# Kernel optimization log

Hardware: AMD Instinct MI355X
Metric: run time of the kernel (lower is better)

Reference implementation:

```python
import jax, jax.numpy as jnp
import numpy as np

M, N, P, T = 8000, 63, 64, 5


def setup_inputs() -> dict:
    key = jax.random.key(0)
    ks = jax.random.split(key, 19)
    sn = (1.0 / N) ** 0.5
    sp = (1.0 / P) ** 0.5
    f32 = jnp.float32
    return {
        "A": jax.random.normal(ks[0], (1, M, N), f32),
        "b": jax.random.normal(ks[1], (1, M), f32),
        "c": jax.random.normal(ks[2], (1, N), f32),
        "theta1r": sn * jax.random.normal(ks[3], (P, N + 1), f32),
        "theta1c": sn * jax.random.normal(ks[4], (P, N + 1), f32),
        "theta2rr": sp * jax.random.normal(ks[5], (P, P), f32),
        "theta2rc": sp * jax.random.normal(ks[6], (P, P), f32),
        "theta2cr": sp * jax.random.normal(ks[7], (P, P), f32),
        "theta3rr": sp * jax.random.normal(ks[8], (P, P), f32),
        "theta3rc": sp * jax.random.normal(ks[9], (P, P), f32),
        "theta3cr": sp * jax.random.normal(ks[10], (P, P), f32),
        "theta4rr": sp * jax.random.normal(ks[11], (P,), f32),
        "theta4rc": sp * jax.random.normal(ks[12], (P,), f32),
        "theta4cr": sp * jax.random.normal(ks[13], (P,), f32),
        "theta6r": sp * jax.random.normal(ks[14], (P, P), f32),
        "theta6c": sp * jax.random.normal(ks[15], (P, P), f32),
        "theta7": sp * jax.random.normal(ks[16], (P, P), f32),
        "W8": 0.05 * jax.random.normal(ks[17], (2, 2 * P), f32),
        "b8": 0.05 * jax.random.normal(ks[18], (2,), f32),
        "z": 7,
    }


def reference(A, b, c, theta1r, theta1c, theta2rr, theta2rc, theta2cr,
              theta3rr, theta3rc, theta3cr, theta4rr, theta4rc, theta4cr,
              theta6r, theta6c, theta7, W8, b8, z):
    relu = jax.nn.relu
    m, n = A.shape[1], A.shape[2]
    p = theta1r.shape[0]
    # raw node features: row node v -> [A[v,:], b[v]]; column node m -> [c, 0]
    Fr_raw = jnp.concatenate([A[0], b[0][:, None]], axis=1)        # (m, n+1)
    fc_raw = jnp.concatenate([c[0], jnp.zeros((1,), A.dtype)])     # (n+1,)
    Fr = Fr_raw / jnp.linalg.norm(Fr_raw, axis=1, keepdims=True)   # f(v), v < m
    fc = fc_raw / jnp.linalg.norm(fc_raw)                          # f(m)
    # edge weights w(v,u) = f(v).f(u) are detached in the original (float(...data))
    Frd = jax.lax.stop_gradient(Fr)
    fcd = jax.lax.stop_gradient(fc)
    Wrr = Frd @ Frd.T                                              # (m, m)
    dg = jnp.diagonal(Wrr)
    srr_pos = relu(Wrr).sum(axis=1) - relu(dg)                     # sum over u != v
    srr_neg = relu(-Wrr).sum(axis=1) - relu(-dg)
    wrc = Frd @ fcd                                                # (m,) = w(v, m)
    # identity: sum_u relu(t4 * w_u) = relu(t4) * sum_u relu(w_u) + relu(-t4) * sum_u relu(-w_u)
    Srr = relu(theta4rr)[:, None] * srr_pos[None, :] + relu(-theta4rr)[:, None] * srr_neg[None, :]
    Src = relu(theta4rc)[:, None] * relu(wrc)[None, :] + relu(-theta4rc)[:, None] * relu(-wrc)[None, :]
    scr = relu(theta4cr) * relu(wrc).sum() + relu(-theta4cr) * relu(-wrc).sum()
    edge_r = theta3rr @ Srr + theta3rc @ Src                       # (p, m), constant over t
    edge_c = theta3cr @ scr                                        # (p,)
    fz = Fr[z]                                                     # z < m: row node feature
    t1r = theta1r @ fz                                             # (p,)
    t1c = theta1c @ fz
    # mu init (p, m+1) = [[Ab^T, c0^T]; 0]; split into row columns / column node
    mu_r0 = jnp.zeros((p, m), A.dtype).at[: n + 1].set(Fr_raw.T)
    mu_c0 = jnp.zeros((p,), A.dtype).at[: n + 1].set(fc_raw)

    def step(carry, _):
        mu_r, mu_c = carry
        # row nodes: term2rr uses old mu[:, v]; term2rc uses old mu[:, m]
        new_r = relu(t1r[:, None] + theta2rr @ mu_r + (theta2rc @ mu_c)[:, None] + edge_r)
        # column node updated last within a sweep -> sees updated row embeddings
        new_c = relu(t1c + theta2cr @ new_r.sum(axis=1) + edge_c)
        return (new_r, new_c), None

    (mu_r, mu_c), _ = jax.lax.scan(step, (mu_r0, mu_c0), None, length=T)
    term6 = theta6r @ mu_r.sum(axis=1) + theta6c @ mu_c            # (p,)
    term7 = theta7 @ mu_r[:, z]                                    # (p,)
    feat = jax.nn.sigmoid(jnp.concatenate([term6, term7]))         # (2p,)
    return (feat @ W8.T + b8)[None, :]                             # (1, 2)
```

## Files before the change

### kernel.cpp

```cpp
#include <hip/hip_runtime.h>
#include <math.h>

typedef __attribute__((ext_vector_type(8))) short short8;
typedef __attribute__((ext_vector_type(4))) float f32x4;

#define WS_SPART 0
#define WS_GPART 262144
#define WS_WPART 294912
#define WS_CPART 295936
#define WS_T1R   336896
#define WS_T1C   336960
#define WS_AL    337024
#define WS_BE    337088
#define WS_GA    337152
#define WS_DE    337216
#define WS_ECP   337280
#define WS_ECN   337344
#define WS_W     337408
#define WS_MUZ   337472
#define WS_WSUM  337536
#define WS_RNORM 337600
#define WS_R2H   345792
#define WS_R2L   347840
#define WS_FLAG  349888
#define WS_FH    380928
#define WS_FL    643072

#define NBLK 125

__device__ __forceinline__ float waveReduceSum(float v) {
#pragma unroll
    for (int m = 32; m >= 1; m >>= 1) v += __shfl_xor(v, m, 64);
    return v;
}
__device__ __forceinline__ unsigned short f2bf(float f) {
    unsigned int u = __float_as_uint(f);
    unsigned int r = (u + 0x7fffu + ((u >> 16) & 1u)) >> 16;
    return (unsigned short)r;
}
__device__ __forceinline__ float bf2f(unsigned short h) {
    return __uint_as_float(((unsigned int)h) << 16);
}

__device__ __forceinline__ float sum32_coherent(const float* base) {
    float v[32];
#pragma unroll
    for (int i = 0; i < 32; i++)
        asm volatile("global_load_dword %0, %1, off sc0 sc1"
                     : "=v"(v[i]) : "v"(base + i * 256));
    asm volatile("s_waitcnt vmcnt(0)" ::: "memory");
    __builtin_amdgcn_sched_barrier(0);
    float s = 0.f;
#pragma unroll
    for (int i = 0; i < 32; i++) s += v[i];
    return s;
}

__device__ __forceinline__ void pollFlags(const int* fb, int lane) {
    for (;;) {
        int f0, f1;
        asm volatile("global_load_dword %0, %1, off sc0 sc1"
                     : "=v"(f0) : "v"(fb + lane));
        asm volatile("global_load_dword %0, %1, off sc0 sc1"
                     : "=v"(f1) : "v"(fb + 64 + lane));
        asm volatile("s_waitcnt vmcnt(0)" : "+v"(f0), "+v"(f1) :: "memory");
        __builtin_amdgcn_sched_barrier(0);
        if (__all((f0 == 1) && (f1 == 1))) return;
        __builtin_amdgcn_s_sleep(1);
    }
}

__global__ __launch_bounds__(256) void k_fr(
    const float* __restrict__ A, const float* __restrict__ b, const float* __restrict__ c,
    const float* __restrict__ th1r, const float* __restrict__ th1c,
    const float* __restrict__ th2rr, const float* __restrict__ th2rc,
    const float* __restrict__ th3rr, const float* __restrict__ th3rc, const float* __restrict__ th3cr,
    const float* __restrict__ th4rr, const float* __restrict__ th4rc, const float* __restrict__ th4cr,
    const int* __restrict__ zp,
    unsigned short* __restrict__ Fh, unsigned short* __restrict__ Fl,
    unsigned short* __restrict__ R2H, unsigned short* __restrict__ R2L,
    float* __restrict__ ws)
{
    int tid = threadIdx.x, lane = tid & 63, wid = tid >> 6;

    if (blockIdx.x == 512) {
        __shared__ float fcraw[64], fz[64], sh4a[64], sh4b[64];
        int p = lane;
        int z = zp[0];
        float cv = (p < 63) ? c[p] : 0.f;
        fcraw[p] = cv;
        float av = (p < 63) ? A[z * 63 + p] : b[z];
        float s2 = waveReduceSum(av * av);
        fz[p] = av * rsqrtf(s2);
        __syncthreads();

        float t1 = 0.f, t2 = 0.f, w0 = 0.f;
#pragma unroll 8
        for (int k = 0; k < 64; k++) {
            t1 += th1r[p * 64 + k] * fz[k];
            t2 += th1c[p * 64 + k] * fz[k];
            w0 += th2rc[p * 64 + k] * fcraw[k];
        }
        ws[WS_T1R + p] = t1;
        ws[WS_T1C + p] = t2;
        ws[WS_W + p] = t1 + w0;

        sh4a[p] = th4rr[p];
        sh4b[p] = th4rc[p];
        __syncthreads();
        float a = 0.f, bb = 0.f, g = 0.f, d = 0.f;
#pragma unroll 8
        for (int k = 0; k < 64; k++) {
            float t4 = sh4a[k];
            a  += th3rr[p * 64 + k] * fmaxf(t4, 0.f);
            bb += th3rr[p * 64 + k] * fmaxf(-t4, 0.f);
            float t5 = sh4b[k];
            g  += th3rc[p * 64 + k] * fmaxf(t5, 0.f);
            d  += th3rc[p * 64 + k] * fmaxf(-t5, 0.f);
        }
        ws[WS_AL + p] = a; ws[WS_BE + p] = bb;
        ws[WS_GA + p] = g; ws[WS_DE + p] = d;
        __syncthreads();
        sh4a[p] = th4cr[p];
        __syncthreads();
        float e1 = 0.f, e2 = 0.f;
#pragma unroll 8
        for (int k = 0; k < 64; k++) {
            float t6 = sh4a[k];
            e1 += th3cr[p * 64 + k] * fmaxf(t6, 0.f);
            e2 += th3cr[p * 64 + k] * fmaxf(-t6, 0.f);
        }
        ws[WS_ECP + p] = e1; ws[WS_ECN + p] = e2;

        if (tid < 128) {
            int* fl = (int*)(ws + WS_FLAG);
#pragma unroll
            for (int t5 = 0; t5 < 5; t5++)
                fl[t5 * 128 + tid] = (tid >= NBLK) ? 1 : 0;
        }
        if (tid < 192) {
#pragma unroll
            for (int t5 = 0; t5 < 5; t5++)
                ws[WS_CPART + t5 * 8192 + 8000 + tid] = 0.f;
        }

#pragma unroll
        for (int i = 0; i < 16; i++) {
            int idx = tid * 16 + i;
            float f = th2rr[idx];
            unsigned short h = f2bf(f);
            R2H[idx] = h;
            R2L[idx] = f2bf(f - bf2f(h));
        }
        return;
    }

    __shared__ float gsh[64];
    __shared__ float wsh2[2];
    if (tid < 64) gsh[tid] = 0.f;
    if (tid < 2) wsh2[tid] = 0.f;
    __syncthreads();

    float cv = (lane < 63) ? c[lane] : 0.f;
    float cn2 = waveReduceSum(cv * cv);
    float fcnl = cv * rsqrtf(cn2);

    int r0 = blockIdx.x * 16 + wid * 4;
    float gl = 0.f, lp = 0.f, ln = 0.f;
#pragma unroll
    for (int i = 0; i < 4; i++) {
        int r = r0 + i;
        if (r < 8000) {
            float val = (lane < 63) ? A[r * 63 + lane] : b[r];
            float s2 = waveReduceSum(val * val);
            float f = val * rsqrtf(s2);
            unsigned short h = f2bf(f);
            Fh[r * 64 + lane] = h;
            Fl[r * 64 + lane] = f2bf(f - bf2f(h));
            gl += f;
            float w = waveReduceSum(f * fcnl);
            if (lane == 0) {
                ws[WS_RNORM + r] = sqrtf(s2);
                lp += fmaxf(w, 0.f); ln += fmaxf(-w, 0.f);
            }
        } else {
            Fh[r * 64 + lane] = 0;
            Fl[r * 64 + lane] = 0;
        }
    }
    atomicAdd(&gsh[lane], gl);
    if (lane == 0) { atomicAdd(&wsh2[0], lp); atomicAdd(&wsh2[1], ln); }
    __syncthreads();
    if (tid < 64) ws[WS_GPART + blockIdx.x * 64 + tid] = gsh[tid];
    if (tid == 64) ws[WS_WPART + blockIdx.x * 2 + 0] = wsh2[0];
    if (tid == 65) ws[WS_WPART + blockIdx.x * 2 + 1] = wsh2[1];
}

__global__ __launch_bounds__(256) void k_gram(
    const unsigned short* __restrict__ Fh, float* __restrict__ ws)
{
    int tid = threadIdx.x, lane = tid & 63, wid = tid >> 6;
    int m = lane & 15, quad = lane >> 4;
    int vbase = blockIdx.x * 256 + wid * 64;

    short8 AH[8];
#pragma unroll
    for (int pt = 0; pt < 4; pt++)
#pragma unroll
        for (int q = 0; q < 2; q++)
            AH[pt * 2 + q] = *(const short8*)(Fh + (vbase + pt * 16 + m) * 64 + q * 32 + quad * 8);

    float srr[16];
#pragma unroll
    for (int i = 0; i < 16; i++) srr[i] = 0.f;

    const int y = blockIdx.y;
    const int boff = m * 64 + quad * 8;
    short8 B0[2], B1[2];
#pragma unroll
    for (int q = 0; q < 2; q++)
        B0[q] = *(const short8*)(Fh + y * 16 * 64 + boff + q * 32);

#pragma unroll 1
    for (int k2 = 0; k2 < 8; k2++) {
        int jB1 = y + 32 * (2 * k2 + 1);
#pragma unroll
        for (int q = 0; q < 2; q++)
            B1[q] = *(const short8*)(Fh + jB1 * 16 * 64 + boff + q * 32);
#pragma unroll
        for (int pt = 0; pt < 4; pt++) {
            f32x4 a = {0.f, 0.f, 0.f, 0.f};
            a = __builtin_amdgcn_mfma_f32_16x16x32_bf16(AH[pt * 2 + 0], B0[0], a, 0, 0, 0);
            a = __builtin_amdgcn_mfma_f32_16x16x32_bf16(AH[pt * 2 + 1], B0[1], a, 0, 0, 0);
#pragma unroll
            for (int r = 0; r < 4; r++) srr[pt * 4 + r] += fmaxf(a[r], 0.f);
        }
        if (k2 < 7) {
            int jB0 = y + 32 * (2 * k2 + 2);
#pragma unroll
            for (int q = 0; q < 2; q++)
                B0[q] = *(const short8*)(Fh + jB0 * 16 * 64 + boff + q * 32);
        }
#pragma unroll
        for (int pt = 0; pt < 4; pt++) {
            f32x4 a = {0.f, 0.f, 0.f, 0.f};
            a = __builtin_amdgcn_mfma_f32_16x16x32_bf16(AH[pt * 2 + 0], B1[0], a, 0, 0, 0);
            a = __builtin_amdgcn_mfma_f32_16x16x32_bf16(AH[pt * 2 + 1], B1[1], a, 0, 0, 0);
#pragma unroll
            for (int r = 0; r < 4; r++) srr[pt * 4 + r] += fmaxf(a[r], 0.f);
        }
    }
#pragma unroll
    for (int pt = 0; pt < 4; pt++)
#pragma unroll
        for (int r = 0; r < 4; r++) {
            float s = srr[pt * 4 + r];
            s += __shfl_xor(s, 1, 64); s += __shfl_xor(s, 2, 64);
            s += __shfl_xor(s, 4, 64); s += __shfl_xor(s, 8, 64);
            if (m == 0)
                ws[WS_SPART + y * 8192 + vbase + pt * 16 + quad * 4 + r] = s;
        }
}

__global__ __launch_bounds__(256) void k_mu_fused(
    const float* __restrict__ c,
    const float* __restrict__ th2cr, const float* __restrict__ th2rc,
    const float* __restrict__ th6r, const float* __restrict__ th6c,
    const float* __restrict__ th7, const float* __restrict__ W8,
    const float* __restrict__ b8, const int* __restrict__ zp,
    float* __restrict__ ws,
    const unsigned short* __restrict__ Fh, const unsigned short* __restrict__ Fl,
    const unsigned short* __restrict__ R2H, const unsigned short* __restrict__ R2L,
    float* __restrict__ out)
{
    __shared__ float XF[64][68];
    __shared__ unsigned short UHT[64][72], ULT[64][72];
    __shared__ float red[256], colp[256];
    __shared__ __align__(16) float wS[64], alS[64], beS[64], gaS[64], deS[64];
    __shared__ float fcnS[64], gS[64], sprow[64];
    __shared__ __align__(16) float e4sh[256];
    __shared__ float Ssh[64], ysh[64], feat[128], muzS[64];

    int tid = threadIdx.x, lane = tid & 63, wid = tid >> 6;
    int m = lane & 15, quad = lane >> 4;
    int v0 = blockIdx.x * 64;
    int cw = wid * 16 + m;
    int v = v0 + cw;
    int z = zp[0];
    int* flags = (int*)(ws + WS_FLAG);

    short8 RH[8], RL[8];
#pragma unroll
    for (int pt = 0; pt < 4; pt++)
#pragma unroll
        for (int q = 0; q < 2; q++) {
            int off = (pt * 16 + m) * 64 + q * 32 + quad * 8;
            RH[pt * 2 + q] = *(const short8*)(R2H + off);
            RL[pt * 2 + q] = *(const short8*)(R2L + off);
        }

    if (wid == 0) {
        float cv = (lane < 63) ? c[lane] : 0.f;
        float cn2 = waveReduceSum(cv * cv);
        fcnS[lane] = cv * rsqrtf(cn2);
        wS[lane] = ws[WS_W + lane];
    } else if (wid == 1) {
        alS[lane] = ws[WS_AL + lane]; beS[lane] = ws[WS_BE + lane];
        float wp = 0.f;
#pragma unroll
        for (int k = 0; k < 8; k++) wp += ws[WS_WPART + (lane + 64 * k) * 2];
        wp = waveReduceSum(wp);
        if (lane == 0) ws[WS_WSUM] = wp;
    } else if (wid == 2) {
        gaS[lane] = ws[WS_GA + lane]; deS[lane] = ws[WS_DE + lane];
        float wn = 0.f;
#pragma unroll
        for (int k = 0; k < 8; k++) wn += ws[WS_WPART + (lane + 64 * k) * 2 + 1];
        wn = waveReduceSum(wn);
        if (lane == 0) ws[WS_WSUM + 1] = wn;
    }
    float gv = 0.f;
#pragma unroll 32
    for (int bb = 0; bb < 128; bb++) gv += ws[WS_GPART + (wid * 128 + bb) * 64 + lane];
    red[tid] = gv;
    __syncthreads();
    if (tid < 64) gS[tid] = red[tid] + red[64 + tid] + red[128 + tid] + red[192 + tid];
    __syncthreads();
    float sv = 0.f;
#pragma unroll
    for (int y = wid * 8; y < wid * 8 + 8; y++) sv += ws[WS_SPART + y * 8192 + v0 + lane];
    red[tid] = sv;
    __syncthreads();
    if (tid < 64) sprow[tid] = red[tid] + red[64 + tid] + red[128 + tid] + red[192 + tid];
    __syncthreads();

    for (int i2 = 0; i2 < 16; i2++) {
        int i = wid * 16 + i2;
        int vr = v0 + i;
        float fr = bf2f(Fh[vr * 64 + lane]) + bf2f(Fl[vr * 64 + lane]);
        float dw = waveReduceSum(fr * fcnS[lane]);
        float dg = waveReduceSum(fr * gS[lane]);
        if (lane == 0) {
            float spv = sprow[i];
            float4 ee;
            ee.x = spv - 1.0f;
            ee.y = spv - dg;
            ee.z = fmaxf(dw, 0.f);
            ee.w = fmaxf(-dw, 0.f);
            *(float4*)(&e4sh[i * 4]) = ee;
        }
        XF[i][lane] = fr * ws[WS_RNORM + vr];
    }
    __syncthreads();

    short8 BH[2], BL[2];
#pragma unroll
    for (int q = 0; q < 2; q++) {
        float4 f0 = *(const float4*)(&XF[cw][q * 32 + quad * 8]);
        float4 f1 = *(const float4*)(&XF[cw][q * 32 + quad * 8 + 4]);
        float xv[8] = {f0.x, f0.y, f0.z, f0.w, f1.x, f1.y, f1.z, f1.w};
        short8 H, L;
#pragma unroll
        for (int j = 0; j < 8; j++) {
            unsigned short h = f2bf(xv[j]);
            H[j] = (short)h;
            L[j] = (short)f2bf(xv[j] - bf2f(h));
        }
        BH[q] = H; BL[q] = L;
    }
    float4 e = *(const float4*)(&e4sh[cw * 4]);

    for (int t = 0; t < 5; t++) {
        if (t > 0) {
#pragma unroll
            for (int q = 0; q < 2; q++) {
                BH[q] = *(const short8*)(&UHT[cw][q * 32 + quad * 8]);
                BL[q] = *(const short8*)(&ULT[cw][q * 32 + quad * 8]);
            }
        }
        f32x4 acc[4];
#pragma unroll
        for (int pt = 0; pt < 4; pt++) {
            f32x4 a = {0.f, 0.f, 0.f, 0.f};
#pragma unroll
            for (int q = 0; q < 2; q++) {
                a = __builtin_amdgcn_mfma_f32_16x16x32_bf16(RH[pt*2+q], BH[q], a, 0, 0, 0);
                a = __builtin_amdgcn_mfma_f32_16x16x32_bf16(RH[pt*2+q], BL[q], a, 0, 0, 0);
                a = __builtin_amdgcn_mfma_f32_16x16x32_bf16(RL[pt*2+q], BH[q], a, 0, 0, 0);
            }
            acc[pt] = a;
        }

        if (t > 0) {
            if (wid == 0) pollFlags(flags + (t - 1) * 128, lane);
            __syncthreads();
            red[tid] = sum32_coherent(ws + WS_CPART + (t - 1) * 8192 + wid * 64 + lane);
            __syncthreads();
            if (tid < 64) Ssh[tid] = red[tid] + red[64 + tid] + red[128 + tid] + red[192 + tid];
            __syncthreads();
            {
                int p = wid * 16 + m;
                float acc2 = 0.f;
                const float4* rowp = (const float4*)(th2cr + p * 64 + quad * 16);
#pragma unroll
                for (int kk = 0; kk < 4; kk++) {
                    float4 r4 = rowp[kk];
                    acc2 += r4.x * Ssh[quad * 16 + 4 * kk]     + r4.y * Ssh[quad * 16 + 4 * kk + 1]
                          + r4.z * Ssh[quad * 16 + 4 * kk + 2] + r4.w * Ssh[quad * 16 + 4 * kk + 3];
                }
                acc2 += __shfl_xor(acc2, 16, 64);
                acc2 += __shfl_xor(acc2, 32, 64);
                if (quad == 0)
                    ysh[p] = fmaxf(acc2 + ws[WS_T1C + p] + ws[WS_WSUM] * ws[WS_ECP + p]
                                   + ws[WS_WSUM + 1] * ws[WS_ECN + p], 0.f);
            }
            __syncthreads();
            {
                int p = wid * 16 + m;
                float acc2 = 0.f;
                const float4* rowp = (const float4*)(th2rc + p * 64 + quad * 16);
#pragma unroll
                for (int kk = 0; kk < 4; kk++) {
                    float4 r4 = rowp[kk];
                    acc2 += r4.x * ysh[quad * 16 + 4 * kk]     + r4.y * ysh[quad * 16 + 4 * kk + 1]
                          + r4.z * ysh[quad * 16 + 4 * kk + 2] + r4.w * ysh[quad * 16 + 4 * kk + 3];
                }
                acc2 += __shfl_xor(acc2, 16, 64);
                acc2 += __shfl_xor(acc2, 32, 64);
                if (quad == 0) wS[p] = acc2 + ws[WS_T1R + p];
            }
            __syncthreads();
        }

#pragma unroll
        for (int pt = 0; pt < 4; pt++) {
            f32x4 a = acc[pt];
            int pbase = pt * 16 + quad * 4;
            float4 w4 = *(const float4*)(wS + pbase);
            float4 a4 = *(const float4*)(alS + pbase);
            float4 b4 = *(const float4*)(beS + pbase);
            float4 g4 = *(const float4*)(gaS + pbase);
            float4 d4 = *(const float4*)(deS + pbase);
            float u0 = fmaxf(a[0] + w4.x + a4.x*e.x + b4.x*e.y + g4.x*e.z + d4.x*e.w, 0.f);
            float u1 = fmaxf(a[1] + w4.y + a4.y*e.x + b4.y*e.y + g4.y*e.z + d4.y*e.w, 0.f);
            float u2 = fmaxf(a[2] + w4.z + a4.z*e.x + b4.z*e.y + g4.z*e.z + d4.z*e.w, 0.f);
            float u3 = fmaxf(a[3] + w4.w + a4.w*e.x + b4.w*e.y + g4.w*e.z + d4.w*e.w, 0.f);
            if (t < 4) {
                ushort4 h4, l4;
                h4.x = f2bf(u0); l4.x = f2bf(u0 - bf2f(h4.x));
                h4.y = f2bf(u1); l4.y = f2bf(u1 - bf2f(h4.y));
                h4.z = f2bf(u2); l4.z = f2bf(u2 - bf2f(h4.z));
                h4.w = f2bf(u3); l4.w = f2bf(u3 - bf2f(h4.w));
                *(ushort4*)(&UHT[cw][pbase]) = h4;
                *(ushort4*)(&ULT[cw][pbase]) = l4;
            } else if (v == z) {
                __hip_atomic_store(&ws[WS_MUZ + pbase + 0], u0, __ATOMIC_RELAXED, __HIP_MEMORY_SCOPE_AGENT);
                __hip_atomic_store(&ws[WS_MUZ + pbase + 1], u1, __ATOMIC_RELAXED, __HIP_MEMORY_SCOPE_AGENT);
                __hip_atomic_store(&ws[WS_MUZ + pbase + 2], u2, __ATOMIC_RELAXED, __HIP_MEMORY_SCOPE_AGENT);
                __hip_atomic_store(&ws[WS_MUZ + pbase + 3], u3, __ATOMIC_RELAXED, __HIP_MEMORY_SCOPE_AGENT);
            }
            float c0 = u0, c1 = u1, c2 = u2, c3 = u3;
#pragma unroll
            for (int mm = 1; mm < 16; mm <<= 1) {
                c0 += __shfl_xor(c0, mm, 64);
                c1 += __shfl_xor(c1, mm, 64);
                c2 += __shfl_xor(c2, mm, 64);
                c3 += __shfl_xor(c3, mm, 64);
            }
            if (m == 0) {
                colp[wid * 64 + pbase + 0] = c0;
                colp[wid * 64 + pbase + 1] = c1;
                colp[wid * 64 + pbase + 2] = c2;
                colp[wid * 64 + pbase + 3] = c3;
            }
        }
        __syncthreads();
        if (tid < 64)
            __hip_atomic_store(&ws[WS_CPART + t * 8192 + blockIdx.x * 64 + tid],
                               colp[tid] + colp[64 + tid] + colp[128 + tid] + colp[192 + tid],
                               __ATOMIC_RELAXED, __HIP_MEMORY_SCOPE_AGENT);
        __syncthreads();
        if (tid == 0) {
            asm volatile("s_waitcnt vmcnt(0)" ::: "memory");
            __hip_atomic_store(&flags[t * 128 + (int)blockIdx.x], 1,
                               __ATOMIC_RELAXED, __HIP_MEMORY_SCOPE_AGENT);
        }
    }

    if (blockIdx.x != 0) return;

    if (wid == 0) pollFlags(flags + 4 * 128, lane);
    __syncthreads();

    red[tid] = sum32_coherent(ws + WS_CPART + 4 * 8192 + wid * 64 + lane);
    if (tid < 64) {
        float mz;
        asm volatile("global_load_dword %0, %1, off sc0 sc1"
                     : "=v"(mz) : "v"(ws + WS_MUZ + tid));
        asm volatile("s_waitcnt vmcnt(0)" : "+v"(mz) :: "memory");
        __builtin_amdgcn_sched_barrier(0);
        muzS[tid] = mz;
    }
    __syncthreads();
    if (tid < 64) Ssh[tid] = red[tid] + red[64 + tid] + red[128 + tid] + red[192 + tid];
    __syncthreads();
    int p = tid;
    if (p < 64) {
        float acc2 = ws[WS_T1C + p] + ws[WS_WSUM] * ws[WS_ECP + p]
                   + ws[WS_WSUM + 1] * ws[WS_ECN + p];
#pragma unroll 8
        for (int k = 0; k < 64; k++) acc2 += th2cr[p * 64 + k] * Ssh[k];
        ysh[p] = fmaxf(acc2, 0.f);
    }
    __syncthreads();
    if (p < 64) {
        float t6 = 0.f, t7 = 0.f;
#pragma unroll 8
        for (int k = 0; k < 64; k++) {
            t6 += th6r[p * 64 + k] * Ssh[k] + th6c[p * 64 + k] * ysh[k];
            t7 += th7[p * 64 + k] * muzS[k];
        }
        feat[p] = 1.f / (1.f + expf(-t6));
        feat[64 + p] = 1.f / (1.f + expf(-t7));
    }
    __syncthreads();
    if (p < 2) {
        float o = b8[p];
        for (int i = 0; i < 128; i++) o += W8[p * 128 + i] * feat[i];
        out[p] = o;
    }
}

extern "C" void kernel_launch(void* const* d_in, const int* in_sizes, int n_in,
                              void* d_out, int out_size, void* d_ws, size_t ws_size,
                              hipStream_t stream) {
    (void)in_sizes; (void)n_in; (void)out_size; (void)ws_size;
    const float* A     = (const float*)d_in[0];
    const float* b     = (const float*)d_in[1];
    const float* c     = (const float*)d_in[2];
    const float* th1r  = (const float*)d_in[3];
    const float* th1c  = (const float*)d_in[4];
    const float* th2rr = (const float*)d_in[5];
    const float* th2rc = (const float*)d_in[6];
    const float* th2cr = (const float*)d_in[7];
    const float* th3rr = (const float*)d_in[8];
    const float* th3rc = (const float*)d_in[9];
    const float* th3cr = (const float*)d_in[10];
    const float* th4rr = (const float*)d_in[11];
    const float* th4rc = (const float*)d_in[12];
    const float* th4cr = (const float*)d_in[13];
    const float* th6r  = (const float*)d_in[14];
    const float* th6c  = (const float*)d_in[15];
    const float* th7   = (const float*)d_in[16];
    const float* W8    = (const float*)d_in[17];
    const float* b8    = (const float*)d_in[18];
    const int*   zp    = (const int*)d_in[19];
    float* ws  = (float*)d_ws;
    float* out = (float*)d_out;
    unsigned short* Fh  = (unsigned short*)(ws + WS_FH);
    unsigned short* Fl  = (unsigned short*)(ws + WS_FL);
    unsigned short* R2H = (unsigned short*)(ws + WS_R2H);
    unsigned short* R2L = (unsigned short*)(ws + WS_R2L);

    k_fr<<<513, 256, 0, stream>>>(A, b, c, th1r, th1c, th2rr, th2rc, th3rr, th3rc,
                                  th3cr, th4rr, th4rc, th4cr, zp, Fh, Fl, R2H, R2L, ws);
    k_gram<<<dim3(32, 32), 256, 0, stream>>>(Fh, ws);
    {
        const unsigned short* Fhc = Fh;
        const unsigned short* Flc = Fl;
        const unsigned short* R2Hc = R2H;
        const unsigned short* R2Lc = R2L;
        void* kargs[] = {
            (void*)&c, (void*)&th2cr, (void*)&th2rc, (void*)&th6r, (void*)&th6c,
            (void*)&th7, (void*)&W8, (void*)&b8, (void*)&zp, (void*)&ws,
            (void*)&Fhc, (void*)&Flc, (void*)&R2Hc, (void*)&R2Lc, (void*)&out };
        hipLaunchCooperativeKernel((const void*)k_mu_fused, dim3(NBLK), dim3(256),
                                   kargs, 0, stream);
    }
}
```

Measured before the change: 227.4 us.

## Exploit Gram symmetry in k_gram and hoist reductions out of mu kernel

The Gram kernel now computes only upper-triangle tiles. Off-diagonal tiles also produce column sums, which are written as the transposed partial row sums, so roughly half the MFMA work is skipped. An otherwise idle lower-triangle block precomputes the global feature sum and the positive and negative weight sums, removing those reductions from the mu kernel's prologue. The theta2 rows and per-row scalars are also preloaded into registers before the time loop. This relies on the launch grid staying at square tile dimensions and adds register pressure in the mu kernel.

```diff
diff --git a/kernel.cpp b/kernel.cpp
--- a/kernel.cpp
+++ b/kernel.cpp
@@ -23,6 +23,7 @@
 #define WS_R2H   345792
 #define WS_R2L   347840
 #define WS_FLAG  349888
+#define WS_GS    350528
 #define WS_FH    380928
 #define WS_FL    643072
 
@@ -199,9 +200,41 @@
 __global__ __launch_bounds__(256) void k_gram(
     const unsigned short* __restrict__ Fh, float* __restrict__ ws)
 {
+    __shared__ float red[256];
+    __shared__ float colw[4][16][16];
     int tid = threadIdx.x, lane = tid & 63, wid = tid >> 6;
     int m = lane & 15, quad = lane >> 4;
-    int vbase = blockIdx.x * 256 + wid * 64;
+    int tx = blockIdx.x, ty = blockIdx.y;
+
+    if (tx > ty) {
+        if (tx == 1 && ty == 0) {
+            float gv = 0.f;
+#pragma unroll 32
+            for (int bb = 0; bb < 128; bb++)
+                gv += ws[WS_GPART + (wid * 128 + bb) * 64 + lane];
+            red[tid] = gv;
+            if (wid == 1) {
+                float wp = 0.f;
+#pragma unroll
+                for (int k = 0; k < 8; k++) wp += ws[WS_WPART + (lane + 64 * k) * 2];
+                wp = waveReduceSum(wp);
+                if (lane == 0) ws[WS_WSUM] = wp;
+            } else if (wid == 2) {
+                float wn = 0.f;
+#pragma unroll
+                for (int k = 0; k < 8; k++) wn += ws[WS_WPART + (lane + 64 * k) * 2 + 1];
+                wn = waveReduceSum(wn);
+                if (lane == 0) ws[WS_WSUM + 1] = wn;
+            }
+            __syncthreads();
+            if (tid < 64)
+                ws[WS_GS + tid] = red[tid] + red[64 + tid] + red[128 + tid] + red[192 + tid];
+        }
+        return;
+    }
+
+    int vbase = tx * 256 + wid * 64;
+    int ubase = ty * 256;
 
     short8 AH[8];
 #pragma unroll
@@ -214,42 +247,58 @@
 #pragma unroll
     for (int i = 0; i < 16; i++) srr[i] = 0.f;
 
-    const int y = blockIdx.y;
     const int boff = m * 64 + quad * 8;
+    const int ub = ubase * 64;
     short8 B0[2], B1[2];
 #pragma unroll
     for (int q = 0; q < 2; q++)
-        B0[q] = *(const short8*)(Fh + y * 16 * 64 + boff + q * 32);
+        B0[q] = *(const short8*)(Fh + ub + boff + q * 32);
 
 #pragma unroll 1
     for (int k2 = 0; k2 < 8; k2++) {
-        int jB1 = y + 32 * (2 * k2 + 1);
 #pragma unroll
         for (int q = 0; q < 2; q++)
-            B1[q] = *(const short8*)(Fh + jB1 * 16 * 64 + boff + q * 32);
-#pragma unroll
-        for (int pt = 0; pt < 4; pt++) {
-            f32x4 a = {0.f, 0.f, 0.f, 0.f};
-            a = __builtin_amdgcn_mfma_f32_16x16x32_bf16(AH[pt * 2 + 0], B0[0], a, 0, 0, 0);
-            a = __builtin_amdgcn_mfma_f32_16x16x32_bf16(AH[pt * 2 + 1], B0[1], a, 0, 0, 0);
-#pragma unroll
-            for (int r = 0; r < 4; r++) srr[pt * 4 + r] += fmaxf(a[r], 0.f);
-        }
-        if (k2 < 7) {
-            int jB0 = y + 32 * (2 * k2 + 2);
+            B1[q] = *(const short8*)(Fh + ub + (2 * k2 + 1) * 1024 + boff + q * 32);
+        {
+            float cs = 0.f;
+#pragma unroll
+            for (int pt = 0; pt < 4; pt++) {
+                f32x4 a = {0.f, 0.f, 0.f, 0.f};
+                a = __builtin_amdgcn_mfma_f32_16x16x32_bf16(AH[pt * 2 + 0], B0[0], a, 0, 0, 0);
+                a = __builtin_amdgcn_mfma_f32_16x16x32_bf16(AH[pt * 2 + 1], B0[1], a, 0, 0, 0);
+#pragma unroll
+                for (int r = 0; r < 4; r++) {
+                    float rr = fmaxf(a[r], 0.f);
+                    srr[pt * 4 + r] += rr; cs += rr;
+                }
+            }
+            cs += __shfl_xor(cs, 16, 64);
+            cs += __shfl_xor(cs, 32, 64);
+            if (quad == 0) colw[wid][2 * k2][m] = cs;
+        }
+        if (k2 < 7)
 #pragma unroll
             for (int q = 0; q < 2; q++)
-                B0[q] = *(const short8*)(Fh + jB0 * 16 * 64 + boff + q * 32);
-        }
-#pragma unroll
-        for (int pt = 0; pt < 4; pt++) {
-            f32x4 a = {0.f, 0.f, 0.f, 0.f};
-            a = __builtin_amdgcn_mfma_f32_16x16x32_bf16(AH[pt * 2 + 0], B1[0], a, 0, 0, 0);
-            a = __builtin_amdgcn_mfma_f32_16x16x32_bf16(AH[pt * 2 + 1], B1[1], a, 0, 0, 0);
-#pragma unroll
-            for (int r = 0; r < 4; r++) srr[pt * 4 + r] += fmaxf(a[r], 0.f);
-        }
-    }
+                B0[q] = *(const short8*)(Fh + ub + (2 * k2 + 2) * 1024 + boff + q * 32);
+        {
+            float cs = 0.f;
+#pragma unroll
+            for (int pt = 0; pt < 4; pt++) {
+                f32x4 a = {0.f, 0.f, 0.f, 0.f};
+                a = __builtin_amdgcn_mfma_f32_16x16x32_bf16(AH[pt * 2 + 0], B1[0], a, 0, 0, 0);
+                a = __builtin_amdgcn_mfma_f32_16x16x32_bf16(AH[pt * 2 + 1], B1[1], a, 0, 0, 0);
+#pragma unroll
+                for (int r = 0; r < 4; r++) {
+                    float rr = fmaxf(a[r], 0.f);
+                    srr[pt * 4 + r] += rr; cs += rr;
+                }
+            }
+            cs += __shfl_xor(cs, 16, 64);
+            cs += __shfl_xor(cs, 32, 64);
+            if (quad == 0) colw[wid][2 * k2 + 1][m] = cs;
+        }
+    }
+    __syncthreads();
 #pragma unroll
     for (int pt = 0; pt < 4; pt++)
 #pragma unroll
@@ -258,8 +307,13 @@
             s += __shfl_xor(s, 1, 64); s += __shfl_xor(s, 2, 64);
             s += __shfl_xor(s, 4, 64); s += __shfl_xor(s, 8, 64);
             if (m == 0)
-                ws[WS_SPART + y * 8192 + vbase + pt * 16 + quad * 4 + r] = s;
-        }
+                ws[WS_SPART + ty * 8192 + vbase + pt * 16 + quad * 4 + r] = s;
+        }
+    if (tx < ty) {
+        float csum = colw[0][tid >> 4][tid & 15] + colw[1][tid >> 4][tid & 15]
+                   + colw[2][tid >> 4][tid & 15] + colw[3][tid >> 4][tid & 15];
+        ws[WS_SPART + tx * 8192 + ubase + tid] = csum;
+    }
 }
 
 __global__ __launch_bounds__(256) void k_mu_fused(
@@ -299,6 +353,17 @@
             RL[pt * 2 + q] = *(const short8*)(R2L + off);
         }
 
+    int prow = wid * 16 + m;
+    float4 Tcr[4], Trc[4];
+#pragma unroll
+    for (int kk = 0; kk < 4; kk++) {
+        Tcr[kk] = ((const float4*)(th2cr + prow * 64 + quad * 16))[kk];
+        Trc[kk] = ((const float4*)(th2rc + prow * 64 + quad * 16))[kk];
+    }
+    float t1c_r = ws[WS_T1C + prow], t1r_r = ws[WS_T1R + prow];
+    float ecp_r = ws[WS_ECP + prow], ecn_r = ws[WS_ECN + prow];
+    float wsp = ws[WS_WSUM], wsn = ws[WS_WSUM + 1];
+
     if (wid == 0) {
         float cv = (lane < 63) ? c[lane] : 0.f;
         float cn2 = waveReduceSum(cv * cv);
@@ -306,26 +371,11 @@
         wS[lane] = ws[WS_W + lane];
     } else if (wid == 1) {
         alS[lane] = ws[WS_AL + lane]; beS[lane] = ws[WS_BE + lane];
-        float wp = 0.f;
-#pragma unroll
-        for (int k = 0; k < 8; k++) wp += ws[WS_WPART + (lane + 64 * k) * 2];
-        wp = waveReduceSum(wp);
-        if (lane == 0) ws[WS_WSUM] = wp;
     } else if (wid == 2) {
         gaS[lane] = ws[WS_GA + lane]; deS[lane] = ws[WS_DE + lane];
-        float wn = 0.f;
-#pragma unroll
-        for (int k = 0; k < 8; k++) wn += ws[WS_WPART + (lane + 64 * k) * 2 + 1];
-        wn = waveReduceSum(wn);
-        if (lane == 0) ws[WS_WSUM + 1] = wn;
-    }
-    float gv = 0.f;
-#pragma unroll 32
-    for (int bb = 0; bb < 128; bb++) gv += ws[WS_GPART + (wid * 128 + bb) * 64 + lane];
-    red[tid] = gv;
-    __syncthreads();
-    if (tid < 64) gS[tid] = red[tid] + red[64 + tid] + red[128 + tid] + red[192 + tid];
-    __syncthreads();
+    } else {
+        gS[lane] = ws[WS_GS + lane];
+    }
     float sv = 0.f;
 #pragma unroll
     for (int y = wid * 8; y < wid * 8 + 8; y++) sv += ws[WS_SPART + y * 8192 + v0 + lane];
@@ -399,35 +449,30 @@
             if (tid < 64) Ssh[tid] = red[tid] + red[64 + tid] + red[128 + tid] + red[192 + tid];
             __syncthreads();
             {
-                int p = wid * 16 + m;
                 float acc2 = 0.f;
-                const float4* rowp = (const float4*)(th2cr + p * 64 + quad * 16);
 #pragma unroll
                 for (int kk = 0; kk < 4; kk++) {
-                    float4 r4 = rowp[kk];
+                    float4 r4 = Tcr[kk];
                     acc2 += r4.x * Ssh[quad * 16 + 4 * kk]     + r4.y * Ssh[quad * 16 + 4 * kk + 1]
                           + r4.z * Ssh[quad * 16 + 4 * kk + 2] + r4.w * Ssh[quad * 16 + 4 * kk + 3];
                 }
                 acc2 += __shfl_xor(acc2, 16, 64);
                 acc2 += __shfl_xor(acc2, 32, 64);
                 if (quad == 0)
-                    ysh[p] = fmaxf(acc2 + ws[WS_T1C + p] + ws[WS_WSUM] * ws[WS_ECP + p]
-                                   + ws[WS_WSUM + 1] * ws[WS_ECN + p], 0.f);
+                    ysh[prow] = fmaxf(acc2 + t1c_r + wsp * ecp_r + wsn * ecn_r, 0.f);
             }
             __syncthreads();
             {
-                int p = wid * 16 + m;
                 float acc2 = 0.f;
-                const float4* rowp = (const float4*)(th2rc + p * 64 + quad * 16);
 #pragma unroll
                 for (int kk = 0; kk < 4; kk++) {
-                    float4 r4 = rowp[kk];
+                    float4 r4 = Trc[kk];
                     acc2 += r4.x * ysh[quad * 16 + 4 * kk]     + r4.y * ysh[quad * 16 + 4 * kk + 1]
                           + r4.z * ysh[quad * 16 + 4 * kk + 2] + r4.w * ysh[quad * 16 + 4 * kk + 3];
                 }
                 acc2 += __shfl_xor(acc2, 16, 64);
                 acc2 += __shfl_xor(acc2, 32, 64);
-                if (quad == 0) wS[p] = acc2 + ws[WS_T1R + p];
+                if (quad == 0) wS[prow] = acc2 + t1r_r;
             }
             __syncthreads();
         }
```

Measured after the change: 218.4 us, median of 3. 3.9% less time.
